# Kernel tuning notes

Hardware: AMD Instinct MI355X
Metric: run time of the kernel (lower is better)

Reference implementation:

```python
import jax, jax.numpy as jnp
import numpy as np

K = 20
EPS = 1e-5
DILATIONS = (1, 2, 4)


def _bn(x, g, b, m, v):
    # inference-mode BatchNorm1d (eval: running stats)
    return (x - m) / jnp.sqrt(v + EPS) * g + b


def _dilated_adj(x, dilation, k):
    B, N, _ = x.shape
    sq = jnp.sum(x * x, axis=-1)
    # squared pairwise distance: monotonic in p=2 cdist -> identical topk indices
    dist2 = sq[:, :, None] + sq[:, None, :] - 2.0 * jnp.einsum('bnc,bmc->bnm', x, x)
    dk = min(k * dilation, N - 1)
    _, idx = jax.lax.top_k(-dist2, dk + 1)          # smallest distances
    sampled = idx[:, :, 1::dilation][:, :, :k]      # skip self, dilated sample (B,N,k)
    bidx = jnp.arange(B)[:, None, None]
    ridx = jnp.arange(N)[None, :, None]
    return jnp.zeros((B, N, N), x.dtype).at[bidx, ridx, sampled].set(1.0)


def _normalize(adj):
    # add self loops then symmetric normalization D^-1/2 (A+I) D^-1/2
    N = adj.shape[1]
    a = adj + jnp.eye(N, dtype=adj.dtype)
    dinv = 1.0 / jnp.sqrt(jnp.sum(a, axis=2))       # degrees >= 1, no inf
    return dinv[:, :, None] * a * dinv[:, None, :]


def _gcn_layer(x, adj, W, b, g, bb, m, v):
    h = x @ W + b                                   # (B,N,Cout)
    h = jnp.einsum('bnm,bmc->bnc', adj, h)          # dense aggregation (bmm)
    return jax.nn.relu(_bn(h, g, bb, m, v))         # dropout is identity in eval


def _forward(x, Wg0, bg0, g0g, g0b, g0m, g0v, Wg1, bg1, g1g, g1b, g1m, g1v, Wg2, bg2, g2g, g2b, g2m, g2v, W1, b1, n1g, n1b, n1m, n1v, W2, b2, n2g, n2b, n2m, n2v, W3, b3, n3g, n3b, n3m, n3v, W4, b4, n4g, n4b, n4m, n4v, W5, b5, n5g, n5b, n5m, n5v, W6, b6):
    gcn_params = ((Wg0, bg0, g0g, g0b, g0m, g0v),
                  (Wg1, bg1, g1g, g1b, g1m, g1v),
                  (Wg2, bg2, g2g, g2b, g2m, g2v))
    feats = x
    ms = []
    for (W, b, g, bb, m, v), dil in zip(gcn_params, DILATIONS):
        adj = _normalize(_dilated_adj(feats, dil, K))
        feats = _gcn_layer(feats, adj, W, b, g, bb, m, v)
        ms.append(feats)
    f = jnp.stack(ms, axis=-1).mean(axis=-1)        # multi-scale mean (B,N,64)
    f = jax.nn.relu(_bn(f @ W1 + b1, n1g, n1b, n1m, n1v))
    f = jax.nn.relu(_bn(f @ W2 + b2, n2g, n2b, n2m, n2v))
    f = jax.nn.relu(_bn(f @ W3 + b3, n3g, n3b, n3m, n3v))
    f = jnp.max(f, axis=1)                          # MaxPool1d(N) over points -> (B,1024)
    f = jax.nn.relu(_bn(f @ W4 + b4, n4g, n4b, n4m, n4v))
    f = jax.nn.relu(_bn(f @ W5 + b5, n5g, n5b, n5m, n5v))
    return f @ W6 + b6                              # (B,40)


def setup_inputs():
    key = jax.random.key(0)
    ks = iter(jax.random.split(key, 32))
    d = {'x': jax.random.normal(next(ks), (32, 1024, 3), jnp.float32)}

    def lin(wn, bn_, ci, co):
        d[wn] = jax.random.normal(next(ks), (ci, co), jnp.float32) * 0.05
        d[bn_] = jnp.zeros((co,), jnp.float32)

    def bnp(p, c):
        d[p + 'g'] = jnp.ones((c,), jnp.float32)
        d[p + 'b'] = jnp.zeros((c,), jnp.float32)
        d[p + 'm'] = jnp.zeros((c,), jnp.float32)
        d[p + 'v'] = jnp.ones((c,), jnp.float32)

    for i, (ci, co) in enumerate(((3, 64), (64, 64), (64, 64))):
        lin('Wg%d' % i, 'bg%d' % i, ci, co)
        bnp('g%d' % i, co)
    for i, (ci, co) in enumerate(((64, 128), (128, 512), (512, 1024), (1024, 1024), (1024, 512)), start=1):
        lin('W%d' % i, 'b%d' % i, ci, co)
        bnp('n%d' % i, co)
    lin('W6', 'b6', 512, 40)
    return d


def reference(x, Wg0, bg0, g0g, g0b, g0m, g0v, Wg1, bg1, g1g, g1b, g1m, g1v, Wg2, bg2, g2g, g2b, g2m, g2v, W1, b1, n1g, n1b, n1m, n1v, W2, b2, n2g, n2b, n2m, n2v, W3, b3, n3g, n3b, n3m, n3v, W4, b4, n4g, n4b, n4m, n4v, W5, b5, n5g, n5b, n5m, n5v, W6, b6):
    return _forward(x, Wg0, bg0, g0g, g0b, g0m, g0v, Wg1, bg1, g1g, g1b, g1m, g1v, Wg2, bg2, g2g, g2b, g2m, g2v, W1, b1, n1g, n1b, n1m, n1v, W2, b2, n2g, n2b, n2m, n2v, W3, b3, n3g, n3b, n3m, n3v, W4, b4, n4g, n4b, n4m, n4v, W5, b5, n5g, n5b, n5m, n5v, W6, b6)
```

## Files before the change

### kernel.cpp

```cpp
#include <hip/hip_runtime.h>
#include <stdint.h>

#define KNN_K 20
#define EPSBN 1e-5f

typedef __attribute__((ext_vector_type(4))) float f32x4;
typedef __attribute__((ext_vector_type(8))) short s16x8;
typedef __attribute__((ext_vector_type(4))) short s16x4;

__device__ __forceinline__ unsigned sortable_f32(float f) {
    unsigned u = __float_as_uint(f);
    return (u & 0x80000000u) ? ~u : (u | 0x80000000u);
}

__device__ __forceinline__ short f2bf(float x) {
    unsigned u = __float_as_uint(x);
    unsigned r = (u + 0x7fffu + ((u >> 16) & 1u)) >> 16;
    return (short)r;
}
__device__ __forceinline__ float bf2f(short h) {
    return __uint_as_float(((unsigned)(unsigned short)h) << 16);
}

__global__ void sq_kernel(const float* __restrict__ x, float* __restrict__ sq,
                          int total, int C) {
    int i = blockIdx.x * 256 + threadIdx.x;
    if (i >= total) return;
    const float* p = x + (size_t)i * C;
    float s = 0.f;
    for (int c = 0; c < C; ++c) s += p[c] * p[c];
    sq[i] = s;
}

__global__ __launch_bounds__(256) void dist128t_kernel(
    const float* __restrict__ feats, const float* __restrict__ sq,
    float* __restrict__ dist, int b0, int N, int C)
{
    int lb = blockIdx.z;
    int b = b0 + lb;
    const float* F = feats + (size_t)b * N * C;
    const float* S = sq + (size_t)b * N;
    float* D = dist + (size_t)lb * N * N;
    int t = blockIdx.x, bi = 0;
    while (t >= 8 - bi) { t -= 8 - bi; ++bi; }
    int bj = bi + t;
    int n0 = bi * 128, m0 = bj * 128;

    __shared__ float As[16][132];
    __shared__ float Bs[16][132];
    int tx = threadIdx.x & 15, ty = threadIdx.x >> 4;
    int tid = threadIdx.x;
    float acc[8][8] = {};
    for (int k0 = 0; k0 < C; k0 += 16) {
        #pragma unroll
        for (int it = 0; it < 8; ++it) {
            int idx = tid + it * 256;
            int r = idx >> 4, kk = idx & 15;
            int gk = k0 + kk;
            As[kk][r] = (gk < C) ? F[(size_t)(n0 + r) * C + gk] : 0.f;
            Bs[kk][r] = (gk < C) ? F[(size_t)(m0 + r) * C + gk] : 0.f;
        }
        __syncthreads();
        #pragma unroll
        for (int kk = 0; kk < 16; ++kk) {
            float4 a0 = *reinterpret_cast<const float4*>(&As[kk][ty * 4]);
            float4 a1 = *reinterpret_cast<const float4*>(&As[kk][64 + ty * 4]);
            float4 b0 = *reinterpret_cast<const float4*>(&Bs[kk][tx * 4]);
            float4 b1 = *reinterpret_cast<const float4*>(&Bs[kk][64 + tx * 4]);
            float av[8] = {a0.x, a0.y, a0.z, a0.w, a1.x, a1.y, a1.z, a1.w};
            float bv[8] = {b0.x, b0.y, b0.z, b0.w, b1.x, b1.y, b1.z, b1.w};
            #pragma unroll
            for (int i = 0; i < 8; ++i)
                #pragma unroll
                for (int j = 0; j < 8; ++j)
                    acc[i][j] = fmaf(av[i], bv[j], acc[i][j]);
        }
        __syncthreads();
    }
    #pragma unroll
    for (int i = 0; i < 8; ++i) {
        int n = n0 + ((i < 4) ? ty * 4 + i : 64 + ty * 4 + (i - 4));
        float sn = S[n];
        #pragma unroll
        for (int j = 0; j < 8; ++j) {
            int m = m0 + ((j < 4) ? tx * 4 + j : 64 + tx * 4 + (j - 4));
            D[(size_t)n * N + m] = (sn + S[m]) - 2.0f * acc[i][j];
        }
    }
    if (bi < bj) {
        #pragma unroll
        for (int j = 0; j < 8; ++j) {
            int m = m0 + ((j < 4) ? tx * 4 + j : 64 + tx * 4 + (j - 4));
            float sm = S[m];
            #pragma unroll
            for (int i = 0; i < 8; ++i) {
                int n = n0 + ((i < 4) ? ty * 4 + i : 64 + ty * 4 + (i - 4));
                D[(size_t)m * N + n] = (sm + S[n]) - 2.0f * acc[i][j];
            }
        }
    }
}

__global__ __launch_bounds__(256) void knn_agg_kernel(
    const float* __restrict__ dist, const float* __restrict__ lin,
    const float* __restrict__ gam, const float* __restrict__ bet,
    const float* __restrict__ mu, const float* __restrict__ var,
    float* __restrict__ feats_out, float* __restrict__ ms,
    short* __restrict__ msh, short* __restrict__ msl,
    int b0, int N, int dil, int mode)
{
    __shared__ alignas(16) unsigned hist[2048];
    __shared__ unsigned long long cand[256];
    __shared__ int nbrs[KNN_K];
    __shared__ float aggP[4][64];
    __shared__ int wsum[4];
    __shared__ int svC0, svP, svD, svCounter;

    int t = threadIdx.x;
    int lb = blockIdx.x / N;
    int n = blockIdx.x - lb * N;
    int b = b0 + lb;
    const int R = KNN_K * dil + 1;

    const float* drow = dist + ((size_t)lb * N + n) * N;
    unsigned long long myk[4];
    #pragma unroll
    for (int s = 0; s < 4; ++s) {
        int m = t + 256 * s;
        float dv = drow[m];
        myk[s] = ((unsigned long long)sortable_f32(dv) << 32) | (unsigned)m;
    }
    #pragma unroll
    for (int h = 0; h < 8; ++h) hist[t * 8 + h] = 0u;
    if (t == 0) svCounter = 0;
    __syncthreads();
    #pragma unroll
    for (int s = 0; s < 4; ++s)
        atomicAdd(&hist[(unsigned)(myk[s] >> 53)], 1u);
    __syncthreads();
    int psum = 0;
    #pragma unroll
    for (int h = 0; h < 8; ++h) psum += (int)hist[t * 8 + h];
    int lane = t & 63, wv = t >> 6;
    int val = psum;
    #pragma unroll
    for (int d = 1; d < 64; d <<= 1) {
        int o = __shfl_up(val, d, 64);
        if (lane >= d) val += o;
    }
    if (lane == 63) wsum[wv] = val;
    __syncthreads();
    int prefix = 0;
    for (int i = 0; i < wv; ++i) prefix += wsum[i];
    int incl = val + prefix;
    int excl = incl - psum;
    if (excl < R && incl >= R) {
        int cum = excl;
        for (int h = 0; h < 8; ++h) {
            int hv = (int)hist[t * 8 + h];
            if (cum + hv >= R) { svD = t * 8 + h; svC0 = cum; svP = hv; break; }
            cum += hv;
        }
    }
    __syncthreads();
    int Cnt = svC0 + svP;
    if (Cnt <= 256) {
        unsigned dpiv = (unsigned)svD;
        #pragma unroll
        for (int s = 0; s < 4; ++s) {
            if ((unsigned)(myk[s] >> 53) <= dpiv) {
                int pos = atomicAdd(&svCounter, 1);
                cand[pos] = myk[s];
            }
        }
        __syncthreads();
        if (t < Cnt) {
            unsigned long long my = cand[t];
            int r = 0;
            for (int c = 0; c < Cnt; ++c) r += (cand[c] < my) ? 1 : 0;
            if (r >= 1) {
                int q = r - 1;
                if (q % dil == 0) {
                    int j = q / dil;
                    if (j < KNN_K) nbrs[j] = (int)(my & 0xFFFFFFFFull);
                }
            }
        }
        __syncthreads();
    } else {
        unsigned long long* keys = (unsigned long long*)hist;
        #pragma unroll
        for (int s = 0; s < 4; ++s) keys[t + 256 * s] = myk[s];
        for (int kk = 2; kk <= 1024; kk <<= 1) {
            for (int jj = kk >> 1; jj > 0; jj >>= 1) {
                __syncthreads();
                #pragma unroll
                for (int s = 0; s < 4; ++s) {
                    int i = t + 256 * s;
                    int ixj = i ^ jj;
                    if (ixj > i) {
                        unsigned long long a = keys[i], c = keys[ixj];
                        bool up = ((i & kk) == 0);
                        if ((a > c) == up) { keys[i] = c; keys[ixj] = a; }
                    }
                }
            }
        }
        __syncthreads();
        if (t < KNN_K) nbrs[t] = (int)(keys[1 + t * dil] & 0xFFFFFFFFull);
        __syncthreads();
    }
    {
        int c = t & 63, g = t >> 6;
        float pacc = 0.f;
        for (int j = g; j < KNN_K; j += 4)
            pacc += lin[((size_t)b * N + nbrs[j]) * 64 + c];
        aggP[g][c] = pacc;
    }
    __syncthreads();
    if (t < 64) {
        const float sc = 1.0f / 21.0f;
        size_t base = ((size_t)b * N + n) * 64;
        float acc = lin[base + t] + aggP[0][t] + aggP[1][t] + aggP[2][t] + aggP[3][t];
        float v = acc * sc;
        v = (v - mu[t]) / sqrtf(var[t] + EPSBN) * gam[t] + bet[t];
        v = fmaxf(v, 0.f);
        if (feats_out) feats_out[base + t] = v;
        if (mode == 0) ms[base + t] = v;
        else if (mode == 1) ms[base + t] += v;
        else {
            float m3 = (ms[base + t] + v) * (1.0f / 3.0f);
            short hh = f2bf(m3);
            msh[base + t] = hh;
            msl[base + t] = f2bf(m3 - bf2f(hh));
        }
    }
}

template<int EPI>
__global__ __launch_bounds__(256) void gemm_kernel(
    const float* __restrict__ A, const float* __restrict__ W,
    const float* __restrict__ bias,
    const float* __restrict__ gam, const float* __restrict__ bet,
    const float* __restrict__ mu, const float* __restrict__ var,
    float* __restrict__ C,
    int M, int K, int N)
{
    __shared__ float As[16][68];
    __shared__ float Bs[16][68];
    int tx = threadIdx.x, ty = threadIdx.y;
    int tid = ty * 16 + tx;
    int row0 = blockIdx.y * 64, col0 = blockIdx.x * 64;
    float acc[4][4] = {};
    for (int k0 = 0; k0 < K; k0 += 16) {
        #pragma unroll
        for (int it = 0; it < 4; ++it) {
            int idx = tid + it * 256;
            int r = idx >> 4, kk = idx & 15;
            int gr = row0 + r, gk = k0 + kk;
            As[kk][r] = (gr < M && gk < K) ? A[(size_t)gr * K + gk] : 0.f;
        }
        #pragma unroll
        for (int it = 0; it < 4; ++it) {
            int idx = tid + it * 256;
            int kk = idx >> 6, c = idx & 63;
            int gk = k0 + kk, gc = col0 + c;
            Bs[kk][c] = (gk < K && gc < N) ? W[(size_t)gk * N + gc] : 0.f;
        }
        __syncthreads();
        #pragma unroll
        for (int kk = 0; kk < 16; ++kk) {
            float4 a4 = *reinterpret_cast<const float4*>(&As[kk][ty * 4]);
            float4 b4 = *reinterpret_cast<const float4*>(&Bs[kk][tx * 4]);
            float av[4] = {a4.x, a4.y, a4.z, a4.w};
            float bv[4] = {b4.x, b4.y, b4.z, b4.w};
            #pragma unroll
            for (int i = 0; i < 4; ++i)
                #pragma unroll
                for (int j = 0; j < 4; ++j)
                    acc[i][j] = fmaf(av[i], bv[j], acc[i][j]);
        }
        __syncthreads();
    }
    #pragma unroll
    for (int i = 0; i < 4; ++i) {
        int r = row0 + ty * 4 + i;
        if (r >= M) break;
        #pragma unroll
        for (int j = 0; j < 4; ++j) {
            int c = col0 + tx * 4 + j;
            if (c >= N) continue;
            float val = acc[i][j] + bias[c];
            if (EPI >= 1) {
                val = (val - mu[c]) / sqrtf(var[c] + EPSBN) * gam[c] + bet[c];
                val = fmaxf(val, 0.f);
            }
            C[(size_t)r * N + c] = val;
        }
    }
}

__global__ __launch_bounds__(256) void skinny_gemm_kernel(
    const float* __restrict__ A, const float* __restrict__ W,
    float* __restrict__ part, int K, int N)
{
    __shared__ float Alds[32][260];
    int tid = threadIdx.x;
    int col0 = blockIdx.x * 32;
    int kc = blockIdx.y;
    int k0 = kc * 256;
    #pragma unroll
    for (int it = 0; it < 8; ++it) {
        int idx = tid + it * 256;
        int r = idx >> 6, kq = (idx & 63) * 4;
        f32x4 v = *(const f32x4*)&A[(size_t)r * K + k0 + kq];
        *(f32x4*)&Alds[r][kq] = v;
    }
    __syncthreads();

    int col = col0 + (tid & 31);
    int g = tid >> 5;
    bool colok = col < N;
    const float* Wp = W + (size_t)k0 * N + (colok ? col : 0);
    float acc0 = 0.f, acc1 = 0.f, acc2 = 0.f, acc3 = 0.f;
    #pragma unroll 4
    for (int k = 0; k < 256; ++k) {
        float wv = Wp[(size_t)k * N];
        acc0 = fmaf(Alds[g * 4 + 0][k], wv, acc0);
        acc1 = fmaf(Alds[g * 4 + 1][k], wv, acc1);
        acc2 = fmaf(Alds[g * 4 + 2][k], wv, acc2);
        acc3 = fmaf(Alds[g * 4 + 3][k], wv, acc3);
    }
    if (colok) {
        size_t base = ((size_t)kc * 32 + g * 4) * N + col;
        part[base]         = acc0;
        part[base + N]     = acc1;
        part[base + 2 * N] = acc2;
        part[base + 3 * N] = acc3;
    }
}

template<int EPI>
__global__ void skinny_reduce_kernel(
    const float* __restrict__ part, const float* __restrict__ bias,
    const float* __restrict__ gam, const float* __restrict__ bet,
    const float* __restrict__ mu, const float* __restrict__ var,
    float* __restrict__ C, int M, int N, int kchunks)
{
    int i = blockIdx.x * 256 + threadIdx.x;
    if (i >= M * N) return;
    int c = i % N;
    float s = 0.f;
    for (int kc = 0; kc < kchunks; ++kc) s += part[(size_t)kc * M * N + i];
    float val = s + bias[c];
    if (EPI >= 1) {
        val = (val - mu[c]) / sqrtf(var[c] + EPSBN) * gam[c] + bet[c];
        val = fmaxf(val, 0.f);
    }
    C[i] = val;
}

__global__ void split_wt_kernel(const float* __restrict__ W,
                                short* __restrict__ Bh, short* __restrict__ Bl,
                                int K, int N)
{
    int n = blockIdx.x * 64 + threadIdx.x;
    if (n >= N) return;
    for (int k0 = 0; k0 < K; k0 += 8) {
        s16x8 h, l;
        #pragma unroll
        for (int e = 0; e < 8; ++e) {
            float x = W[(size_t)(k0 + e) * N + n];
            short hh = f2bf(x);
            h[e] = hh;
            l[e] = f2bf(x - bf2f(hh));
        }
        *(s16x8*)&Bh[(size_t)n * K + k0] = h;
        *(s16x8*)&Bl[(size_t)n * K + k0] = l;
    }
}

template<int EPI>
__global__ __launch_bounds__(256) void gemm_mfma_kernel(
    const short* __restrict__ Ah, const short* __restrict__ Al,
    const short* __restrict__ Bh, const short* __restrict__ Bl,
    const float* __restrict__ bias,
    const float* __restrict__ gam, const float* __restrict__ bet,
    const float* __restrict__ mu, const float* __restrict__ var,
    short* __restrict__ Chi, short* __restrict__ Clo,
    float* __restrict__ pool,
    int M, int K, int N, int rowsPerBatch)
{
    __shared__ short Alds[128][72];
    __shared__ short Blds[128][72];
    __shared__ int poolS[128];

    int tid = threadIdx.x;
    int wave = tid >> 6, lane = tid & 63;
    int wr = wave >> 1, wc = wave & 1;
    int nx = N >> 7;
    int rowsPerXcd = (M >> 7) >> 3;
    int bid = blockIdx.x;
    int xcd = bid & 7, l = bid >> 3;
    int tileY = xcd * rowsPerXcd + l / nx;
    int tileX = l - (l / nx) * nx;
    int row0 = tileY * 128, col0 = tileX * 128;

    int fr = lane & 15, fq = lane >> 4;
    int kb = fq * 8;

    f32x4 acc[4][4] = {};

    for (int k0 = 0; k0 < K; k0 += 32) {
        #pragma unroll
        for (int it = 0; it < 2; ++it) {
            int idx = tid + it * 256;
            int r = idx >> 2, ch = (idx & 3) * 8;
            size_t go = (size_t)(row0 + r) * K + k0 + ch;
            *(s16x8*)&Alds[r][ch]      = *(const s16x8*)&Ah[go];
            *(s16x8*)&Alds[r][32 + ch] = *(const s16x8*)&Al[go];
        }
        #pragma unroll
        for (int it = 0; it < 2; ++it) {
            int idx = tid + it * 256;
            int c = idx >> 2, ch = (idx & 3) * 8;
            size_t bo = (size_t)(col0 + c) * K + k0 + ch;
            *(s16x8*)&Blds[c][ch]      = *(const s16x8*)&Bh[bo];
            *(s16x8*)&Blds[c][32 + ch] = *(const s16x8*)&Bl[bo];
        }
        __syncthreads();

        s16x8 ah[4], al[4], bhf[4], blf[4];
        #pragma unroll
        for (int i = 0; i < 4; ++i) {
            int r = wr * 64 + i * 16 + fr;
            ah[i] = *(const s16x8*)&Alds[r][kb];
            al[i] = *(const s16x8*)&Alds[r][32 + kb];
        }
        #pragma unroll
        for (int j = 0; j < 4; ++j) {
            int c = wc * 64 + j * 16 + fr;
            bhf[j] = *(const s16x8*)&Blds[c][kb];
            blf[j] = *(const s16x8*)&Blds[c][32 + kb];
        }
        #pragma unroll
        for (int i = 0; i < 4; ++i)
            #pragma unroll
            for (int j = 0; j < 4; ++j) {
                acc[i][j] = __builtin_amdgcn_mfma_f32_16x16x32_bf16(ah[i], bhf[j], acc[i][j], 0, 0, 0);
                acc[i][j] = __builtin_amdgcn_mfma_f32_16x16x32_bf16(ah[i], blf[j], acc[i][j], 0, 0, 0);
                acc[i][j] = __builtin_amdgcn_mfma_f32_16x16x32_bf16(al[i], bhf[j], acc[i][j], 0, 0, 0);
            }
        __syncthreads();
    }

    if (EPI == 1) {
        #pragma unroll
        for (int j = 0; j < 4; ++j) {
            int col = col0 + wc * 64 + j * 16 + fr;
            float bs = bias[col], g = gam[col], be = bet[col], m = mu[col];
            float inv = 1.0f / sqrtf(var[col] + EPSBN);
            #pragma unroll
            for (int i = 0; i < 4; ++i) {
                int rbase = row0 + wr * 64 + i * 16 + fq * 4;
                #pragma unroll
                for (int reg = 0; reg < 4; ++reg) {
                    float val = acc[i][j][reg] + bs;
                    val = (val - m) * inv * g + be;
                    val = fmaxf(val, 0.f);
                    short hh = f2bf(val);
                    size_t o = (size_t)(rbase + reg) * N + col;
                    Chi[o] = hh;
                    Clo[o] = f2bf(val - bf2f(hh));
                }
            }
        }
    } else {
        float cmax[4];
        #pragma unroll
        for (int j = 0; j < 4; ++j) {
            int col = col0 + wc * 64 + j * 16 + fr;
            float bs = bias[col], g = gam[col], be = bet[col], m = mu[col];
            float inv = 1.0f / sqrtf(var[col] + EPSBN);
            float cm = 0.f;
            #pragma unroll
            for (int i = 0; i < 4; ++i)
                #pragma unroll
                for (int reg = 0; reg < 4; ++reg) {
                    float val = acc[i][j][reg] + bs;
                    val = (val - m) * inv * g + be;
                    val = fmaxf(val, 0.f);
                    cm = fmaxf(cm, val);
                }
            cmax[j] = cm;
        }
        #pragma unroll
        for (int j = 0; j < 4; ++j) {
            cmax[j] = fmaxf(cmax[j], __shfl_xor(cmax[j], 16, 64));
            cmax[j] = fmaxf(cmax[j], __shfl_xor(cmax[j], 32, 64));
        }
        if (tid < 128) poolS[tid] = 0;
        __syncthreads();
        if (fq == 0) {
            #pragma unroll
            for (int j = 0; j < 4; ++j)
                atomicMax(&poolS[wc * 64 + j * 16 + fr], __float_as_int(cmax[j]));
        }
        __syncthreads();
        if (tid < 128) {
            int bb = row0 / rowsPerBatch;
            atomicMax((int*)&pool[(size_t)bb * N + col0 + tid], poolS[tid]);
        }
    }
}

extern "C" void kernel_launch(void* const* d_in, const int* in_sizes, int n_in,
                              void* d_out, int out_size, void* d_ws, size_t ws_size,
                              hipStream_t stream)
{
    (void)in_sizes; (void)n_in; (void)out_size;
    const int B = 32, N = 1024, MBN = B * N;
    const float* x = (const float*)d_in[0];

    const float *Wg[3], *bg[3], *gg[3], *gb[3], *gm[3], *gv[3];
    for (int i = 0; i < 3; ++i) {
        int base = 1 + i * 6;
        Wg[i] = (const float*)d_in[base + 0];
        bg[i] = (const float*)d_in[base + 1];
        gg[i] = (const float*)d_in[base + 2];
        gb[i] = (const float*)d_in[base + 3];
        gm[i] = (const float*)d_in[base + 4];
        gv[i] = (const float*)d_in[base + 5];
    }
    const float *Wm[5], *bm[5], *ng[5], *nb[5], *nm[5], *nv[5];
    for (int i = 0; i < 5; ++i) {
        int base = 19 + i * 6;
        Wm[i] = (const float*)d_in[base + 0];
        bm[i] = (const float*)d_in[base + 1];
        ng[i] = (const float*)d_in[base + 2];
        nb[i] = (const float*)d_in[base + 3];
        nm[i] = (const float*)d_in[base + 4];
        nv[i] = (const float*)d_in[base + 5];
    }
    const float* W6 = (const float*)d_in[49];
    const float* b6 = (const float*)d_in[50];

    char* w = (char*)d_ws;
    size_t off = 0;
    auto allocB = [&](size_t bytes) {
        void* p = w + off;
        off += (bytes + 255) & ~(size_t)255;
        return p;
    };
    float* ms     = (float*)allocB((size_t)MBN * 64 * 4);
    float* fA     = (float*)allocB((size_t)MBN * 64 * 4);
    float* fB     = (float*)allocB((size_t)MBN * 64 * 4);
    float* lin    = (float*)allocB((size_t)MBN * 64 * 4);
    float* sqv    = (float*)allocB((size_t)MBN * 4);
    float* pooled = (float*)allocB((size_t)B * 1024 * 4);
    float* f4     = (float*)allocB((size_t)B * 1024 * 4);
    float* f5     = (float*)allocB((size_t)B * 512 * 4);
    float* skpart = (float*)allocB((size_t)4 * 32 * 1024 * 4);
    short* msh    = (short*)allocB((size_t)MBN * 64 * 2);
    short* msl    = (short*)allocB((size_t)MBN * 64 * 2);
    short* w1h    = (short*)allocB((size_t)64 * 128 * 2);
    short* w1l    = (short*)allocB((size_t)64 * 128 * 2);
    short* w2h    = (short*)allocB((size_t)128 * 512 * 2);
    short* w2l    = (short*)allocB((size_t)128 * 512 * 2);
    short* w3h    = (short*)allocB((size_t)512 * 1024 * 2);
    short* w3l    = (short*)allocB((size_t)512 * 1024 * 2);
    size_t bigOff = off;
    short* f1h = (short*)(w + bigOff);
    short* f1l = (short*)(w + bigOff + 1 * (size_t)MBN * 128 * 2);
    short* f2h = (short*)(w + bigOff + 2 * (size_t)MBN * 128 * 2);
    short* f2l = (short*)(w + bigOff + 2 * (size_t)MBN * 128 * 2 + (size_t)MBN * 512 * 2);
    float* distB = (float*)(w + bigOff);
    size_t distBytes = (size_t)N * N * sizeof(float);
    int chunkB = 1;
    if (ws_size > bigOff) {
        size_t cap = (ws_size - bigOff) / distBytes;
        chunkB = (int)(cap < 32 ? cap : 32);
        if (chunkB < 1) chunkB = 1;
    }

    dim3 blk16(16, 16);
    auto grid64  = [](int M, int Nn) { return dim3((unsigned)((Nn + 63) / 64), (unsigned)((M + 63) / 64)); };
    auto gridMf1 = [](int M, int Nn) { return dim3((unsigned)((Nn / 128) * (M / 128))); };

    split_wt_kernel<<<dim3(128 / 64), 64, 0, stream>>>(Wm[0], w1h, w1l, 64, 128);
    split_wt_kernel<<<dim3(512 / 64), 64, 0, stream>>>(Wm[1], w2h, w2l, 128, 512);
    split_wt_kernel<<<dim3(1024 / 64), 64, 0, stream>>>(Wm[2], w3h, w3l, 512, 1024);

    const float* featsIn = x;
    float* featsOutArr[3] = { fA, fB, nullptr };
    int Cin[3] = { 3, 64, 64 };
    int dils[3] = { 1, 2, 4 };
    for (int L = 0; L < 3; ++L) {
        sq_kernel<<<(MBN + 255) / 256, 256, 0, stream>>>(featsIn, sqv, MBN, Cin[L]);
        gemm_kernel<0><<<grid64(MBN, 64), blk16, 0, stream>>>(
            featsIn, Wg[L], bg[L], nullptr, nullptr, nullptr, nullptr,
            lin, MBN, Cin[L], 64);
        for (int b0 = 0; b0 < B; b0 += chunkB) {
            int cb = (B - b0 < chunkB) ? (B - b0) : chunkB;
            dist128t_kernel<<<dim3(36, 1, (unsigned)cb), 256, 0, stream>>>(
                featsIn, sqv, distB, b0, N, Cin[L]);
            knn_agg_kernel<<<cb * N, 256, 0, stream>>>(
                distB, lin, gg[L], gb[L], gm[L], gv[L],
                featsOutArr[L], ms, msh, msl, b0, N, dils[L], L);
        }
        featsIn = featsOutArr[L];
    }

    gemm_mfma_kernel<1><<<gridMf1(MBN, 128), 256, 0, stream>>>(
        msh, msl, w1h, w1l, bm[0], ng[0], nb[0], nm[0], nv[0],
        f1h, f1l, nullptr, MBN, 64, 128, N);
    gemm_mfma_kernel<1><<<gridMf1(MBN, 512), 256, 0, stream>>>(
        f1h, f1l, w2h, w2l, bm[1], ng[1], nb[1], nm[1], nv[1],
        f2h, f2l, nullptr, MBN, 128, 512, N);
    hipMemsetAsync(pooled, 0, (size_t)B * 1024 * sizeof(float), stream);
    gemm_mfma_kernel<2><<<gridMf1(MBN, 1024), 256, 0, stream>>>(
        f2h, f2l, w3h, w3l, bm[2], ng[2], nb[2], nm[2], nv[2],
        nullptr, nullptr, pooled, MBN, 512, 1024, N);

    skinny_gemm_kernel<<<dim3(1024 / 32, 4), 256, 0, stream>>>(pooled, Wm[3], skpart, 1024, 1024);
    skinny_reduce_kernel<1><<<(32 * 1024 + 255) / 256, 256, 0, stream>>>(
        skpart, bm[3], ng[3], nb[3], nm[3], nv[3], f4, 32, 1024, 4);
    skinny_gemm_kernel<<<dim3(512 / 32, 4), 256, 0, stream>>>(f4, Wm[4], skpart, 1024, 512);
    skinny_reduce_kernel<1><<<(32 * 512 + 255) / 256, 256, 0, stream>>>(
        skpart, bm[4], ng[4], nb[4], nm[4], nv[4], f5, 32, 512, 4);
    skinny_gemm_kernel<<<dim3(2, 2), 256, 0, stream>>>(f5, W6, skpart, 512, 40);
    skinny_reduce_kernel<0><<<(32 * 40 + 255) / 256, 256, 0, stream>>>(
        skpart, b6, nullptr, nullptr, nullptr, nullptr, (float*)d_out, 32, 40, 2);
}
```

Measured before the change: 761.1 us.

## Process one KNN query row per wavefront instead of per block

Rewrites the KNN select-and-aggregate kernel so each 64-lane wavefront handles one point's distance row, with four rows per 256-thread block. Block-wide __syncthreads are replaced by wave-local shuffles, ballot and __threadfence_block. The histogram is packed as two 16-bit counters per word, loads are vectorized, and the bitonic-sort fallback becomes an iterative wave-min selection. The aim is to cut barrier and launch overhead and raise occupancy. In exchange, each lane does more serial work, and correctness now depends on wave-synchronous execution and on N being divisible by 4.

```diff
diff --git a/kernel.cpp b/kernel.cpp
--- a/kernel.cpp
+++ b/kernel.cpp
@@ -101,7 +101,7 @@
     }
 }
 
-__global__ __launch_bounds__(256) void knn_agg_kernel(
+__global__ __launch_bounds__(256) void knn_agg_wave_kernel(
     const float* __restrict__ dist, const float* __restrict__ lin,
     const float* __restrict__ gam, const float* __restrict__ bet,
     const float* __restrict__ mu, const float* __restrict__ var,
@@ -109,130 +109,167 @@
     short* __restrict__ msh, short* __restrict__ msl,
     int b0, int N, int dil, int mode)
 {
-    __shared__ alignas(16) unsigned hist[2048];
-    __shared__ unsigned long long cand[256];
-    __shared__ int nbrs[KNN_K];
-    __shared__ float aggP[4][64];
-    __shared__ int wsum[4];
-    __shared__ int svC0, svP, svD, svCounter;
-
-    int t = threadIdx.x;
-    int lb = blockIdx.x / N;
-    int n = blockIdx.x - lb * N;
+    __shared__ alignas(16) unsigned hist[4][1024];
+    __shared__ unsigned long long cand[4][256];
+    __shared__ int nbrs[4][KNN_K];
+    __shared__ int cnts[4];
+
+    int tid = threadIdx.x;
+    int wv = tid >> 6, lane = tid & 63;
+    int p = blockIdx.x * 4 + wv;
+    int lb = p / N, n = p - lb * N;
     int b = b0 + lb;
     const int R = KNN_K * dil + 1;
 
     const float* drow = dist + ((size_t)lb * N + n) * N;
-    unsigned long long myk[4];
+    const f32x4* drow4 = (const f32x4*)drow;
+    unsigned long long k[16];
     #pragma unroll
     for (int s = 0; s < 4; ++s) {
-        int m = t + 256 * s;
-        float dv = drow[m];
-        myk[s] = ((unsigned long long)sortable_f32(dv) << 32) | (unsigned)m;
-    }
-    #pragma unroll
-    for (int h = 0; h < 8; ++h) hist[t * 8 + h] = 0u;
-    if (t == 0) svCounter = 0;
-    __syncthreads();
-    #pragma unroll
-    for (int s = 0; s < 4; ++s)
-        atomicAdd(&hist[(unsigned)(myk[s] >> 53)], 1u);
-    __syncthreads();
+        f32x4 v = drow4[s * 64 + lane];
+        #pragma unroll
+        for (int e = 0; e < 4; ++e) {
+            int m = (s * 64 + lane) * 4 + e;
+            k[s * 4 + e] = ((unsigned long long)sortable_f32(v[e]) << 32) | (unsigned)m;
+        }
+    }
+    unsigned* H = hist[wv];
+    {
+        uint4 z = {0u, 0u, 0u, 0u};
+        #pragma unroll
+        for (int i = 0; i < 4; ++i) *(uint4*)&H[lane * 16 + i * 4] = z;
+    }
+    if (lane == 0) cnts[wv] = 0;
+    __threadfence_block();
+    #pragma unroll
+    for (int s = 0; s < 16; ++s) {
+        unsigned d = (unsigned)(k[s] >> 53);
+        atomicAdd(&H[d >> 1], 1u << ((d & 1) << 4));
+    }
+    __threadfence_block();
+    unsigned w[16];
+    #pragma unroll
+    for (int i = 0; i < 4; ++i) *(uint4*)&w[i * 4] = *(const uint4*)&H[lane * 16 + i * 4];
     int psum = 0;
     #pragma unroll
-    for (int h = 0; h < 8; ++h) psum += (int)hist[t * 8 + h];
-    int lane = t & 63, wv = t >> 6;
-    int val = psum;
+    for (int i = 0; i < 16; ++i) psum += (int)(w[i] & 0xFFFFu) + (int)(w[i] >> 16);
+    int incl = psum;
     #pragma unroll
     for (int d = 1; d < 64; d <<= 1) {
-        int o = __shfl_up(val, d, 64);
-        if (lane >= d) val += o;
-    }
-    if (lane == 63) wsum[wv] = val;
-    __syncthreads();
-    int prefix = 0;
-    for (int i = 0; i < wv; ++i) prefix += wsum[i];
-    int incl = val + prefix;
+        int o = __shfl_up(incl, d, 64);
+        if (lane >= d) incl += o;
+    }
     int excl = incl - psum;
-    if (excl < R && incl >= R) {
+    int svDl = 0, c0l = 0, pl = 0;
+    bool found = (excl < R && incl >= R);
+    if (found) {
         int cum = excl;
-        for (int h = 0; h < 8; ++h) {
-            int hv = (int)hist[t * 8 + h];
-            if (cum + hv >= R) { svD = t * 8 + h; svC0 = cum; svP = hv; break; }
+        #pragma unroll
+        for (int i = 0; i < 32; ++i) {
+            int hv = (i & 1) ? (int)(w[i >> 1] >> 16) : (int)(w[i >> 1] & 0xFFFFu);
+            if (cum + hv >= R) { svDl = lane * 32 + i; c0l = cum; pl = hv; break; }
             cum += hv;
         }
     }
-    __syncthreads();
+    unsigned long long fm = __ballot(found);
+    int src = __ffsll(fm) - 1;
+    int svD  = __shfl(svDl, src, 64);
+    int svC0 = __shfl(c0l, src, 64);
+    int svP  = __shfl(pl, src, 64);
     int Cnt = svC0 + svP;
+
     if (Cnt <= 256) {
-        unsigned dpiv = (unsigned)svD;
-        #pragma unroll
-        for (int s = 0; s < 4; ++s) {
-            if ((unsigned)(myk[s] >> 53) <= dpiv) {
-                int pos = atomicAdd(&svCounter, 1);
-                cand[pos] = myk[s];
-            }
-        }
-        __syncthreads();
-        if (t < Cnt) {
-            unsigned long long my = cand[t];
-            int r = 0;
-            for (int c = 0; c < Cnt; ++c) r += (cand[c] < my) ? 1 : 0;
-            if (r >= 1) {
-                int q = r - 1;
-                if (q % dil == 0) {
-                    int j = q / dil;
-                    if (j < KNN_K) nbrs[j] = (int)(my & 0xFFFFFFFFull);
+        #pragma unroll
+        for (int s = 0; s < 16; ++s) {
+            if ((unsigned)(k[s] >> 53) <= (unsigned)svD) {
+                int pos = atomicAdd(&cnts[wv], 1);
+                cand[wv][pos] = k[s];
+            }
+        }
+        __threadfence_block();
+        unsigned long long my[4];
+        #pragma unroll
+        for (int q = 0; q < 4; ++q) {
+            int slot = lane + q * 64;
+            my[q] = (slot < Cnt) ? cand[wv][slot] : ~0ull;
+        }
+        int r0 = 0, r1 = 0, r2 = 0, r3 = 0;
+        for (int c = 0; c < Cnt; ++c) {
+            unsigned long long v = cand[wv][c];
+            r0 += (v < my[0]) ? 1 : 0;
+            r1 += (v < my[1]) ? 1 : 0;
+            r2 += (v < my[2]) ? 1 : 0;
+            r3 += (v < my[3]) ? 1 : 0;
+        }
+        int rr[4] = {r0, r1, r2, r3};
+        #pragma unroll
+        for (int q = 0; q < 4; ++q) {
+            int slot = lane + q * 64;
+            if (slot < Cnt && rr[q] >= 1) {
+                int q2 = rr[q] - 1;
+                if (q2 % dil == 0) {
+                    int j = q2 / dil;
+                    if (j < KNN_K) nbrs[wv][j] = (int)(my[q] & 0xFFFFFFFFull);
                 }
             }
         }
-        __syncthreads();
     } else {
-        unsigned long long* keys = (unsigned long long*)hist;
-        #pragma unroll
-        for (int s = 0; s < 4; ++s) keys[t + 256 * s] = myk[s];
-        for (int kk = 2; kk <= 1024; kk <<= 1) {
-            for (int jj = kk >> 1; jj > 0; jj >>= 1) {
-                __syncthreads();
-                #pragma unroll
-                for (int s = 0; s < 4; ++s) {
-                    int i = t + 256 * s;
-                    int ixj = i ^ jj;
-                    if (ixj > i) {
-                        unsigned long long a = keys[i], c = keys[ixj];
-                        bool up = ((i & kk) == 0);
-                        if ((a > c) == up) { keys[i] = c; keys[ixj] = a; }
-                    }
+        unsigned cm = 0;
+        #pragma unroll
+        for (int s = 0; s < 16; ++s)
+            if ((unsigned)(k[s] >> 53) <= (unsigned)svD) cm |= (1u << s);
+        for (int r = 0; r < R; ++r) {
+            unsigned long long lm = ~0ull;
+            #pragma unroll
+            for (int s = 0; s < 16; ++s)
+                if ((cm >> s) & 1u) lm = (k[s] < lm) ? k[s] : lm;
+            #pragma unroll
+            for (int d = 32; d; d >>= 1) {
+                unsigned long long o = __shfl_xor(lm, d, 64);
+                lm = (o < lm) ? o : lm;
+            }
+            bool done = false;
+            #pragma unroll
+            for (int s = 0; s < 16; ++s) {
+                if (!done && ((cm >> s) & 1u) && k[s] == lm) {
+                    cm &= ~(1u << s);
+                    done = true;
                 }
             }
-        }
-        __syncthreads();
-        if (t < KNN_K) nbrs[t] = (int)(keys[1 + t * dil] & 0xFFFFFFFFull);
-        __syncthreads();
-    }
+            if (r >= 1 && lane == 0) {
+                int q2 = r - 1;
+                if (q2 % dil == 0) {
+                    int j = q2 / dil;
+                    if (j < KNN_K) nbrs[wv][j] = (int)(lm & 0xFFFFFFFFull);
+                }
+            }
+        }
+    }
+    __threadfence_block();
+
     {
-        int c = t & 63, g = t >> 6;
-        float pacc = 0.f;
-        for (int j = g; j < KNN_K; j += 4)
-            pacc += lin[((size_t)b * N + nbrs[j]) * 64 + c];
-        aggP[g][c] = pacc;
-    }
-    __syncthreads();
-    if (t < 64) {
         const float sc = 1.0f / 21.0f;
         size_t base = ((size_t)b * N + n) * 64;
-        float acc = lin[base + t] + aggP[0][t] + aggP[1][t] + aggP[2][t] + aggP[3][t];
+        float part[4];
+        #pragma unroll
+        for (int g = 0; g < 4; ++g) {
+            float pacc = 0.f;
+            for (int j = g; j < KNN_K; j += 4)
+                pacc += lin[((size_t)b * N + nbrs[wv][j]) * 64 + lane];
+            part[g] = pacc;
+        }
+        float acc = lin[base + lane] + part[0] + part[1] + part[2] + part[3];
         float v = acc * sc;
-        v = (v - mu[t]) / sqrtf(var[t] + EPSBN) * gam[t] + bet[t];
+        v = (v - mu[lane]) / sqrtf(var[lane] + EPSBN) * gam[lane] + bet[lane];
         v = fmaxf(v, 0.f);
-        if (feats_out) feats_out[base + t] = v;
-        if (mode == 0) ms[base + t] = v;
-        else if (mode == 1) ms[base + t] += v;
+        if (feats_out) feats_out[base + lane] = v;
+        if (mode == 0) ms[base + lane] = v;
+        else if (mode == 1) ms[base + lane] += v;
         else {
-            float m3 = (ms[base + t] + v) * (1.0f / 3.0f);
+            float m3 = (ms[base + lane] + v) * (1.0f / 3.0f);
             short hh = f2bf(m3);
-            msh[base + t] = hh;
-            msl[base + t] = f2bf(m3 - bf2f(hh));
+            msh[base + lane] = hh;
+            msl[base + lane] = f2bf(m3 - bf2f(hh));
         }
     }
 }
@@ -604,7 +641,7 @@
             int cb = (B - b0 < chunkB) ? (B - b0) : chunkB;
             dist128t_kernel<<<dim3(36, 1, (unsigned)cb), 256, 0, stream>>>(
                 featsIn, sqv, distB, b0, N, Cin[L]);
-            knn_agg_kernel<<<cb * N, 256, 0, stream>>>(
+            knn_agg_wave_kernel<<<cb * N / 4, 256, 0, stream>>>(
                 distB, lin, gg[L], gb[L], gm[L], gv[L],
                 featsOutArr[L], ms, msh, msl, b0, N, dils[L], L);
         }
```

New measurement: 689.0 us, median of 2. 1.1x faster.
